# Kernel optimization log

Measured on AMD Instinct MI355X. Metric: run time of the kernel, lower is better.

Reference implementation:

```python
import math
import jax, jax.numpy as jnp
import numpy as np

HID = 1536; H = 8; D = HID // H           # hidden, heads, head_dim
W = 12                                     # chunk (query block) size
L = 13; R = 0                              # context left / right
MAX_PAST = L - 1; MAX_FUT = R
C = W + MAX_PAST + MAX_FUT                 # key context size per block (24)
F = MAX_PAST + MAX_FUT + 1                 # relative span (13)
CAP = 50.0
B, T = 4, 4096


def _timing_signal(positions):
    # positions: [F] float -> [F, HID] sinusoidal embedding
    num_ts = HID // 2
    log_inc = math.log(10000.0) / max(num_ts - 1, 1)
    inv = jnp.exp(jnp.arange(num_ts, dtype=jnp.float32) * -log_inc)
    scaled = positions[:, None] * inv[None, :]
    return jnp.concatenate([jnp.sin(scaled), jnp.cos(scaled)], axis=-1)


def setup_inputs() -> dict:
    key = jax.random.key(0)
    ks = jax.random.split(key, 6)
    s = HID ** -0.5
    return {
        "hidden_states": jax.random.normal(ks[0], (B, T, HID), jnp.float32),
        "mask": jnp.zeros((B, T), bool),  # True = padded/invalid position
        "wq": jax.random.normal(ks[1], (HID, HID), jnp.float32) * s,
        "wk": jax.random.normal(ks[2], (HID, HID), jnp.float32) * s,
        "wv": jax.random.normal(ks[3], (HID, HID), jnp.float32) * s,
        "w_pos": jax.random.normal(ks[4], (HID, HID), jnp.float32) * s,
        "per_dim_scale": jnp.zeros((D,), jnp.float32),
    }


def reference(hidden_states, mask, wq, wk, wv, w_pos, per_dim_scale):
    Bq, Tq, _ = hidden_states.shape
    U = -(-Tq // W)  # number of query blocks
    q = (hidden_states @ wq).reshape(Bq, Tq, H, D)
    k = (hidden_states @ wk).reshape(Bq, Tq, H, D)
    v = (hidden_states @ wv).reshape(Bq, Tq, H, D)
    # q scaling: head_dim**-0.5 / softplus(0) * softplus(per_dim_scale)
    q_scale = (D ** -0.5) / math.log(2.0)
    q = q * (q_scale * jax.nn.softplus(per_dim_scale))
    # query blocks [B, U, W, H, D]
    qb = jnp.pad(q, ((0, 0), (0, U * W - Tq), (0, 0), (0, 0))).reshape(Bq, U, W, H, D)
    # key/value blocks with left/right context [B, U, C, H, D]
    frame_idx = jnp.arange(U)[:, None] * W + jnp.arange(C)[None, :]

    def extract(x):
        pads = ((0, 0), (MAX_PAST, U * W - Tq + MAX_FUT)) + ((0, 0),) * (x.ndim - 2)
        return jnp.pad(x, pads)[:, frame_idx]

    kb = extract(k)
    vb = extract(v)
    valid = extract(~mask)  # [B, U, C] bool, padded frames -> False
    # relative position embedding: projected sinusoid for offsets [MAX_PAST..-MAX_FUT]
    pos = jnp.arange(MAX_PAST, -MAX_FUT - 1, -1, dtype=jnp.float32)  # [F]
    sin_emb = (_timing_signal(pos) @ w_pos).reshape(F, H, D)
    term_ac = jnp.einsum('buwhd,buchd->bhuwc', qb, kb)   # content logits
    term_bd = jnp.einsum('buwhd,fhd->bhuwf', qb, sin_emb)  # position logits (unshifted)
    # Transformer-XL relative shift: pad last dim to C+1, flatten W*(C+1), keep W*C
    tb = jnp.pad(term_bd, ((0, 0),) * 4 + ((0, C + 1 - F),))
    tb = tb.reshape(Bq, H, U, W * (C + 1))[..., :W * C].reshape(Bq, H, U, W, C)
    logits = jnp.tanh((term_ac + tb) / CAP) * CAP
    # local causal validity mask [W, C]
    lower = jnp.tril(jnp.ones((C, W), bool)).T
    upper = jnp.tril(jnp.ones((W, C), bool), k=MAX_PAST + MAX_FUT)
    cond = valid[:, None, :, None, :] & (lower & upper)[None, None, None]
    logits = jnp.where(cond, logits, jnp.float32(np.finfo(np.float32).min))
    probs = jax.nn.softmax(logits, axis=-1)
    ctx = jnp.einsum('bhuwc,buchd->buwhd', probs, vb)
    return ctx.reshape(Bq, U * W, H, D)[:, :Tq]
```

## Files before the change

### kernel.cpp

```cpp
#include <hip/hip_runtime.h>
#include <hip/hip_bf16.h>
#include <cstdint>
#include <cstddef>

typedef __bf16 bf16x8 __attribute__((ext_vector_type(8)));
typedef __bf16 bf16x4_t __attribute__((ext_vector_type(4)));
typedef float f32x4 __attribute__((ext_vector_type(4)));
using bf16_t = __hip_bfloat16;

constexpr int kHID = 1536;
constexpr int kH = 8;
constexpr int kD = 192;
constexpr int kW = 12;
constexpr int kC = 24;
constexpr int kF = 13;
constexpr int kB = 4;
constexpr int kT = 4096;
constexpr int kU = 342;
constexpr int kNQKV = 4608;
constexpr int kM = kB * kT;
constexpr int kKV = 2 * kHID;

constexpr size_t kVtOff = 50331648;
constexpr size_t kWtOff = 100663296;
constexpr size_t kSinOff = kWtOff + (size_t)kNQKV * kHID * 2;
constexpr size_t kSinBfOff = kSinOff + (size_t)kF * kHID * 4;
constexpr size_t kSsOff = kSinBfOff + (size_t)16 * kHID * 2;
constexpr size_t kHsbOff = kSsOff + 1024;
constexpr size_t kQbOff = kHsbOff + (size_t)kM * kHID * 2;
constexpr size_t kWsNeedSmall = kQbOff;
constexpr size_t kWsNeedBig = kQbOff + (size_t)kM * kHID * 2;

__device__ __forceinline__ void load_lds16(const void* g, void* l) {
  __builtin_amdgcn_global_load_lds(
      (const __attribute__((address_space(1))) void*)g,
      (__attribute__((address_space(3))) void*)l, 16, 0, 0);
}

__global__ __launch_bounds__(256) void transpose_w(const float* __restrict__ wq,
                                                   const float* __restrict__ wk,
                                                   const float* __restrict__ wv,
                                                   bf16_t* __restrict__ wt) {
  __shared__ bf16_t tile[32][33];
  const int s = blockIdx.z;
  const float* w = (s == 0) ? wq : (s == 1) ? wk : wv;
  const int k0 = blockIdx.x * 32, n0 = blockIdx.y * 32;
  for (int i = threadIdx.y; i < 32; i += 8)
    tile[i][threadIdx.x] = (bf16_t)w[(size_t)(k0 + i) * kHID + n0 + threadIdx.x];
  __syncthreads();
  for (int i = threadIdx.y; i < 32; i += 8)
    wt[(size_t)(s * kHID + n0 + i) * kHID + k0 + threadIdx.x] = tile[threadIdx.x][i];
}

__global__ __launch_bounds__(256) void convert_hs(const float* __restrict__ hs,
                                                  bf16_t* __restrict__ hsb) {
  const size_t total = (size_t)kM * kHID;
  const size_t stride = (size_t)gridDim.x * 256 * 8;
  for (size_t i = ((size_t)blockIdx.x * 256 + threadIdx.x) * 8; i < total; i += stride) {
    f32x4 a = *(const f32x4*)(hs + i);
    f32x4 b = *(const f32x4*)(hs + i + 4);
    bf16x8 o;
#pragma unroll
    for (int e = 0; e < 4; e++) { o[e] = (__bf16)a[e]; o[e + 4] = (__bf16)b[e]; }
    *(bf16x8*)(hsb + i) = o;
  }
}

__global__ __launch_bounds__(256) void sinemb_kernel(const float* __restrict__ w_pos,
                                                     float* __restrict__ sinb,
                                                     bf16_t* __restrict__ sinbf) {
  __shared__ float ts[kHID];
  const int f = blockIdx.y;
  const int n = blockIdx.x * 256 + threadIdx.x;
  const float pos = (float)(12 - f);
  const float log_inc = logf(10000.0f) / 767.0f;
  for (int j = threadIdx.x; j < 768; j += 256) {
    float inv = expf(-(float)j * log_inc);
    float a = pos * inv;
    ts[j] = sinf(a);
    ts[768 + j] = cosf(a);
  }
  __syncthreads();
  float acc = 0.0f;
  for (int m = 0; m < kHID; m++) acc += ts[m] * w_pos[(size_t)m * kHID + n];
  sinb[f * kHID + n] = acc;
  sinbf[f * kHID + n] = (bf16_t)acc;
  if (f == 0) {
    sinbf[13 * kHID + n] = (bf16_t)0.0f;
    sinbf[14 * kHID + n] = (bf16_t)0.0f;
    sinbf[15 * kHID + n] = (bf16_t)0.0f;
  }
}

__global__ void compute_ss(const float* __restrict__ pds, float* __restrict__ ssb) {
  int d = threadIdx.x;
  if (d < kD) {
    float p = pds[d];
    float sp = log1pf(expf(p));
    ssb[d] = (1.0f / (sqrtf(192.0f) * logf(2.0f))) * sp;
  }
}

template <int MODE>
__global__ __launch_bounds__(256) void gemm_qkv_t(const bf16_t* __restrict__ hsb,
                                                  const bf16_t* __restrict__ wt,
                                                  float* __restrict__ qout,
                                                  bf16_t* __restrict__ kvout,
                                                  bf16_t* __restrict__ vtws,
                                                  bf16_t* __restrict__ qbout,
                                                  const float* __restrict__ ssb) {
  __shared__ bf16_t As[128 * 32];
  __shared__ bf16_t Bs[128 * 32];
  const int tid = threadIdx.x;
  const int lane = tid & 63, wid = tid >> 6;
  const int t0 = blockIdx.y * 128, n0 = blockIdx.x * 128;
  const int mb = lane & 15, quad = lane >> 4;
  const int wrow = (wid >> 1) * 64, wcol = (wid & 1) * 64;

  f32x4 acc[4][4] = {};

  const int c0 = tid, c1 = tid + 256;
  const bf16_t* a0 = hsb + (size_t)(t0 + (c0 >> 2)) * kHID + (c0 & 3) * 8;
  const bf16_t* a1 = hsb + (size_t)(t0 + (c1 >> 2)) * kHID + (c1 & 3) * 8;
  const bf16_t* b0 = wt + (size_t)(n0 + (c0 >> 2)) * kHID + (c0 & 3) * 8;
  const bf16_t* b1 = wt + (size_t)(n0 + (c1 >> 2)) * kHID + (c1 & 3) * 8;
  bf16_t* lA0 = &As[c0 * 8];
  bf16_t* lA1 = &As[c1 * 8];
  bf16_t* lB0 = &Bs[c0 * 8];
  bf16_t* lB1 = &Bs[c1 * 8];

  for (int k0 = 0; k0 < kHID; k0 += 32) {
    __syncthreads();
    load_lds16(a0, lA0);
    load_lds16(a1, lA1);
    load_lds16(b0, lB0);
    load_lds16(b1, lB1);
    a0 += 32; a1 += 32; b0 += 32; b1 += 32;
    __syncthreads();

    bf16x8 af[4], bg[4];
#pragma unroll
    for (int i = 0; i < 4; i++)
      af[i] = *(const bf16x8*)(&As[(wrow + i * 16 + mb) * 32 + quad * 8]);
#pragma unroll
    for (int j = 0; j < 4; j++)
      bg[j] = *(const bf16x8*)(&Bs[(wcol + j * 16 + mb) * 32 + quad * 8]);
#pragma unroll
    for (int i = 0; i < 4; i++)
#pragma unroll
      for (int j = 0; j < 4; j++)
        acc[i][j] = __builtin_amdgcn_mfma_f32_16x16x32_bf16(af[i], bg[j], acc[i][j], 0, 0, 0);
  }

  if constexpr (MODE == 0) {
    const bool isq = (n0 < kHID);
#pragma unroll
    for (int i = 0; i < 4; i++)
#pragma unroll
      for (int j = 0; j < 4; j++)
#pragma unroll
        for (int r = 0; r < 4; r++) {
          int row = t0 + wrow + i * 16 + quad * 4 + r;
          int col = wcol + j * 16 + mb;
          if (isq) {
            qout[(size_t)row * kHID + n0 + col] = acc[i][j][r];
          } else {
            kvout[(size_t)row * kKV + (n0 - kHID) + col] = (bf16_t)acc[i][j][r];
          }
        }
  } else {
    if (n0 < kHID) {
#pragma unroll
      for (int j = 0; j < 4; j++) {
        int colj = n0 + wcol + j * 16 + mb;
        float ssv = ssb[colj % kD];
#pragma unroll
        for (int i = 0; i < 4; i++)
#pragma unroll
          for (int r = 0; r < 4; r++) {
            int row = t0 + wrow + i * 16 + quad * 4 + r;
            qbout[(size_t)row * kHID + colj] = (bf16_t)(acc[i][j][r] * ssv);
          }
      }
    } else if (n0 < 2 * kHID) {
#pragma unroll
      for (int i = 0; i < 4; i++)
#pragma unroll
        for (int j = 0; j < 4; j++)
#pragma unroll
          for (int r = 0; r < 4; r++) {
            int row = t0 + wrow + i * 16 + quad * 4 + r;
            int col = (n0 - kHID) + wcol + j * 16 + mb;
            kvout[(size_t)row * kHID + col] = (bf16_t)acc[i][j][r];
          }
    } else {
#pragma unroll
      for (int i = 0; i < 4; i++)
#pragma unroll
        for (int j = 0; j < 4; j++) {
          int vcol = (n0 - 2 * kHID) + wcol + j * 16 + mb;
          int row = t0 + wrow + i * 16 + quad * 4;
          bf16x4_t vv;
#pragma unroll
          for (int r = 0; r < 4; r++) vv[r] = (__bf16)acc[i][j][r];
          *(bf16x4_t*)(vtws + (size_t)vcol * kM + row) = vv;
        }
    }
  }
}

__global__ __launch_bounds__(256) void attn_mfma(const bf16_t* __restrict__ kvK,
                                                 const bf16_t* __restrict__ vtws,
                                                 const unsigned char* __restrict__ mask,
                                                 const bf16_t* __restrict__ sinbf,
                                                 const bf16_t* __restrict__ qb,
                                                 float* __restrict__ out) {
  const int g = blockIdx.x, b = blockIdx.y, h = blockIdx.z;
  const int tid = threadIdx.x;
  const int lane = tid & 63, wv = tid >> 6;
  const int w = lane & 15, quad = lane >> 4;
  const int tb = g * 48 - 12;
  const int u = g * 4 + wv;

  __shared__ bf16_t Ks[68 * 192];
  __shared__ bf16_t Vt[192 * 80];
  __shared__ __align__(16) char scr[4][1280];
  __shared__ int vld[68];

  float* bdl = (float*)scr[wv];
  bf16_t* Pl = (bf16_t*)scr[wv];

  int tq = u * kW + w;
  int qrow = (u < kU && tq < kT) ? (b * kT + tq) : (b * kT);
  const bf16_t* qptr = qb + (size_t)qrow * kHID + h * kD + quad * 8;
  const bf16_t* sptr = sinbf + (size_t)w * kHID + h * kD + quad * 8;
  bf16x8 qf[6], sf[6];
#pragma unroll
  for (int ks = 0; ks < 6; ks++) {
    qf[ks] = *(const bf16x8*)(qptr + ks * 32);
    sf[ks] = *(const bf16x8*)(sptr + ks * 32);
  }

  if (tid < 68) {
    int p = tb + tid;
    vld[tid] = (p >= 0 && p < kT && mask[b * kT + p] == 0) ? 1 : 0;
  }

  const char* kvb = (const char*)kvK;
#pragma unroll
  for (int it = 0; it < 7; it++) {
    int i = it * 256 + tid;
    if (i >= 1632) i -= 1632;
    int r = i / 24, cb = (i % 24) * 16;
    int row = b * kT + tb + r;
    row = row < 0 ? 0 : (row > kM - 1 ? kM - 1 : row);
    const char* src = kvb + (size_t)row * 3072 + h * 384 + (cb ^ ((r & 7) << 4));
    load_lds16(src, (char*)Ks + i * 16);
  }
  const char* vtb = (const char*)vtws;
#pragma unroll
  for (int it = 0; it < 8; it++) {
    int i = it * 256 + tid;
    if (i >= 1920) i -= 1920;
    int d = i / 10, j = i % 10;
    int e = b * kT + tb - 4 + j * 8;
    e = e < 0 ? 0 : (e > kM - 8 ? kM - 8 : e);
    const char* src = vtb + ((size_t)(h * kD + d) * kM + e) * 2;
    load_lds16(src, (char*)Vt + i * 16);
  }
  __syncthreads();

  f32x4 ac0 = {0.f, 0.f, 0.f, 0.f}, ac1 = {0.f, 0.f, 0.f, 0.f}, bdv = {0.f, 0.f, 0.f, 0.f};
  const int r0 = wv * kW + w;
  const int r1 = r0 + 16;
#pragma unroll
  for (int ks = 0; ks < 6; ks++) {
    int kb = ks * 64 + quad * 16;
    bf16x8 ka0 = *(const bf16x8*)((const char*)Ks + (size_t)r0 * 384 + (kb ^ ((r0 & 7) << 4)));
    bf16x8 ka1 = *(const bf16x8*)((const char*)Ks + (size_t)r1 * 384 + (kb ^ ((r1 & 7) << 4)));
    ac0 = __builtin_amdgcn_mfma_f32_16x16x32_bf16(ka0, qf[ks], ac0, 0, 0, 0);
    ac1 = __builtin_amdgcn_mfma_f32_16x16x32_bf16(ka1, qf[ks], ac1, 0, 0, 0);
    bdv = __builtin_amdgcn_mfma_f32_16x16x32_bf16(sf[ks], qf[ks], bdv, 0, 0, 0);
  }

  *(f32x4*)&bdl[w * 16 + quad * 4] = bdv;
  asm volatile("s_waitcnt lgkmcnt(0)" ::: "memory");

  float l[8];
#pragma unroll
  for (int T = 0; T < 2; T++)
#pragma unroll
    for (int r = 0; r < 4; r++) {
      int c = T * 16 + quad * 4 + r;
      int f = c - w;
      int fr = f < 0 ? 0 : (f > 15 ? 15 : f);
      float a = T ? ac1[r] : ac0[r];
      float bb = bdl[w * 16 + fr];
      bool val = (f >= 0) && (f <= 12) && (c < kC) && (vld[wv * kW + c] != 0);
      float x2 = (a + bb) * 0.04f;
      float ee = __expf(x2);
      float th = (ee - 1.0f) * __builtin_amdgcn_rcpf(ee + 1.0f);
      l[T * 4 + r] = val ? 50.0f * th : -3.4028234663852886e38f;
    }

  float m = l[0];
#pragma unroll
  for (int k = 1; k < 8; k++) m = fmaxf(m, l[k]);
  m = fmaxf(m, __shfl_xor(m, 16, 64));
  m = fmaxf(m, __shfl_xor(m, 32, 64));
  float e8[8], s = 0.0f;
#pragma unroll
  for (int k = 0; k < 8; k++) { e8[k] = __expf(l[k] - m); s += e8[k]; }
  s += __shfl_xor(s, 16, 64);
  s += __shfl_xor(s, 32, 64);
  float inv = 1.0f / s;

#pragma unroll
  for (int T = 0; T < 2; T++) {
    bf16x4_t pk;
#pragma unroll
    for (int r = 0; r < 4; r++) {
      int c = T * 16 + quad * 4 + r;
      float p = (c < kC) ? e8[T * 4 + r] * inv : 0.0f;
      pk[r] = (__bf16)p;
    }
    *(bf16x4_t*)&Pl[w * 40 + T * 16 + quad * 4] = pk;
  }
  asm volatile("s_waitcnt lgkmcnt(0)" ::: "memory");
  __builtin_amdgcn_sched_barrier(0);

  bf16x8 pa = *(const bf16x8*)&Pl[w * 40 + quad * 8];
  const int cl0 = 4 + wv * kW + quad * 8;
  const bool uok = (u < kU);
#pragma unroll
  for (int T = 0; T < 12; T++) {
    bf16x4_t v0 = *(const bf16x4_t*)&Vt[(T * 16 + w) * 80 + cl0];
    bf16x4_t v1 = *(const bf16x4_t*)&Vt[(T * 16 + w) * 80 + cl0 + 4];
    bf16x8 vf;
#pragma unroll
    for (int e2 = 0; e2 < 4; e2++) { vf[e2] = v0[e2]; vf[e2 + 4] = v1[e2]; }
    f32x4 oz = {0.f, 0.f, 0.f, 0.f};
    oz = __builtin_amdgcn_mfma_f32_16x16x32_bf16(pa, vf, oz, 0, 0, 0);
    if (uok) {
#pragma unroll
      for (int r = 0; r < 4; r++) {
        int wr = quad * 4 + r;
        int t = u * kW + wr;
        if (wr < kW && t < kT)
          out[((size_t)(b * kT + t)) * kHID + h * kD + T * 16 + w] = oz[r];
      }
    }
  }
}

__global__ __launch_bounds__(256) void attn_kernel(const bf16_t* __restrict__ kv,
                                                   const unsigned char* __restrict__ mask,
                                                   const float* __restrict__ sinb,
                                                   const float* __restrict__ pds,
                                                   float* __restrict__ out) {
  const int u = blockIdx.x, b = blockIdx.y, h = blockIdx.z;
  const int tid = threadIdx.x;

  __shared__ float qs[kW][kD + 1];
  __shared__ float ks[kC][kD + 1];
  __shared__ float vs[kC][kD + 1];
  __shared__ float sins[kF][kD + 1];
  __shared__ float lg[kW][kC + 1];
  __shared__ float ss[kD];
  __shared__ int validc[kC];

  if (tid < kD) {
    float p = pds[tid];
    float sp = log1pf(expf(p));
    ss[tid] = (1.0f / (sqrtf(192.0f) * logf(2.0f))) * sp;
  }
  if (tid < kC) {
    int p = u * kW + tid - 12;
    validc[tid] = (p >= 0 && p < kT && mask[b * kT + p] == 0) ? 1 : 0;
  }
  __syncthreads();

  for (int i = tid; i < kW * kD; i += 256) {
    int w = i / kD, d = i % kD;
    int t = u * kW + w;
    float v = 0.0f;
    if (t < kT) v = out[((size_t)(b * kT + t)) * kHID + h * kD + d] * ss[d];
    qs[w][d] = v;
  }
  for (int i = tid; i < kC * kD; i += 256) {
    int c = i / kD, d = i % kD;
    int p = u * kW + c - 12;
    float kval = 0.0f, vval = 0.0f;
    if (p >= 0 && p < kT) {
      size_t base = (size_t)(b * kT + p) * kKV;
      kval = (float)kv[base + h * kD + d];
      vval = (float)kv[base + kHID + h * kD + d];
    }
    ks[c][d] = kval;
    vs[c][d] = vval;
  }
  for (int i = tid; i < kF * kD; i += 256) {
    int f = i / kD, d = i % kD;
    sins[f][d] = sinb[f * kHID + h * kD + d];
  }
  __syncthreads();

  for (int i = tid; i < kW * kC; i += 256) {
    int w = i / kC, c = i % kC;
    float l = -3.4028234663852886e38f;
    int f = c - w;
    if (f >= 0 && f <= 12 && validc[c]) {
      float ac = 0.0f, bd = 0.0f;
      for (int d = 0; d < kD; d++) {
        float q = qs[w][d];
        ac += q * ks[c][d];
        bd += q * sins[f][d];
      }
      l = tanhf((ac + bd) * (1.0f / 50.0f)) * 50.0f;
    }
    lg[w][c] = l;
  }
  __syncthreads();

  if (tid < kW) {
    float m = -3.4028234663852886e38f;
#pragma unroll
    for (int c = 0; c < kC; c++) m = fmaxf(m, lg[tid][c]);
    float e[kC];
    float s = 0.0f;
#pragma unroll
    for (int c = 0; c < kC; c++) {
      float ex = expf(lg[tid][c] - m);
      e[c] = ex;
      s += ex;
    }
    float inv = 1.0f / s;
#pragma unroll
    for (int c = 0; c < kC; c++) lg[tid][c] = e[c] * inv;
  }
  __syncthreads();

  for (int i = tid; i < kW * kD; i += 256) {
    int w = i / kD, d = i % kD;
    int t = u * kW + w;
    if (t >= kT) continue;
    float acc = 0.0f;
#pragma unroll
    for (int c = 0; c < 13; c++) acc += lg[w][w + c] * vs[w + c][d];
    out[((size_t)(b * kT + t)) * kHID + h * kD + d] = acc;
  }
}

extern "C" void kernel_launch(void* const* d_in, const int* in_sizes, int n_in,
                              void* d_out, int out_size, void* d_ws, size_t ws_size,
                              hipStream_t stream) {
  if (ws_size < kWsNeedSmall) return;

  const float* hs = (const float*)d_in[0];
  const unsigned char* mask = (const unsigned char*)d_in[1];
  const float* wq = (const float*)d_in[2];
  const float* wk = (const float*)d_in[3];
  const float* wv = (const float*)d_in[4];
  const float* wpos = (const float*)d_in[5];
  const float* pds = (const float*)d_in[6];
  float* out = (float*)d_out;

  char* ws = (char*)d_ws;
  bf16_t* kvK = (bf16_t*)ws;
  bf16_t* vtws = (bf16_t*)(ws + kVtOff);
  bf16_t* wt = (bf16_t*)(ws + kWtOff);
  float* sinb = (float*)(ws + kSinOff);
  bf16_t* sinbf = (bf16_t*)(ws + kSinBfOff);
  float* ssb = (float*)(ws + kSsOff);
  bf16_t* hsb = (bf16_t*)(ws + kHsbOff);
  bf16_t* qb = (bf16_t*)(ws + kQbOff);

  const bool big = ws_size >= kWsNeedBig;

  transpose_w<<<dim3(48, 48, 3), dim3(32, 8), 0, stream>>>(wq, wk, wv, wt);
  convert_hs<<<dim3(2048), 256, 0, stream>>>(hs, hsb);
  sinemb_kernel<<<dim3(6, 13), 256, 0, stream>>>(wpos, sinb, sinbf);
  compute_ss<<<1, 192, 0, stream>>>(pds, ssb);

  if (big) {
    gemm_qkv_t<1><<<dim3(kNQKV / 128, kM / 128), 256, 0, stream>>>(
        hsb, wt, nullptr, kvK, vtws, qb, ssb);
    attn_mfma<<<dim3(86, kB, kH), 256, 0, stream>>>(kvK, vtws, mask, sinbf, qb, out);
  } else {
    gemm_qkv_t<0><<<dim3(kNQKV / 128, kM / 128), 256, 0, stream>>>(
        hsb, wt, out, kvK, nullptr, nullptr, nullptr);
    attn_kernel<<<dim3(kU, kB, kH), 256, 0, stream>>>(kvK, mask, sinb, pds, out);
  }
}
```

Baseline: 611.7 us.

## Add 256x256-tile QKV GEMM with 128KB LDS and split-K sinusoid projection

Adds a new QKV projection GEMM that uses 256x256 output tiles, 512 threads, 128KB of dynamic LDS, swizzled async LDS staging and double buffering. Larger tiles raise arithmetic intensity and cut how often operands are reloaded from global memory. It falls back to the old 128-tile GEMM if the attribute set or launch fails. Separately, the serial 1536-step sinusoid-embedding matvec is split across 12 K-chunks (written temporarily into the output buffer) followed by a reduce kernel, which adds parallelism to that small stage.

```diff
diff --git a/kernel.cpp b/kernel.cpp
--- a/kernel.cpp
+++ b/kernel.cpp
@@ -85,6 +85,52 @@
   for (int m = 0; m < kHID; m++) acc += ts[m] * w_pos[(size_t)m * kHID + n];
   sinb[f * kHID + n] = acc;
   sinbf[f * kHID + n] = (bf16_t)acc;
+  if (f == 0) {
+    sinbf[13 * kHID + n] = (bf16_t)0.0f;
+    sinbf[14 * kHID + n] = (bf16_t)0.0f;
+    sinbf[15 * kHID + n] = (bf16_t)0.0f;
+  }
+}
+
+__global__ __launch_bounds__(256) void sinemb_part(const float* __restrict__ w_pos,
+                                                   float* __restrict__ sinp) {
+  __shared__ float tsL[kF][128];
+  const int nc = blockIdx.x;
+  const int ms = blockIdx.y;
+  const int tid = threadIdx.x;
+  const float log_inc = logf(10000.0f) / 767.0f;
+  for (int i = tid; i < kF * 128; i += 256) {
+    int f = i >> 7, ml = i & 127;
+    int m = ms * 128 + ml;
+    float pos = (float)(12 - f);
+    float v;
+    if (m < 768) v = sinf(pos * expf(-(float)m * log_inc));
+    else v = cosf(pos * expf(-(float)(m - 768) * log_inc));
+    tsL[f][ml] = v;
+  }
+  __syncthreads();
+  const int n = nc * 256 + tid;
+  float acc[kF] = {};
+  for (int ml = 0; ml < 128; ml++) {
+    float wp = w_pos[(size_t)(ms * 128 + ml) * kHID + n];
+#pragma unroll
+    for (int f = 0; f < kF; f++) acc[f] += tsL[f][ml] * wp;
+  }
+#pragma unroll
+  for (int f = 0; f < kF; f++) sinp[((size_t)ms * kF + f) * kHID + n] = acc[f];
+}
+
+__global__ __launch_bounds__(256) void sinemb_reduce(const float* __restrict__ sinp,
+                                                     float* __restrict__ sinb,
+                                                     bf16_t* __restrict__ sinbf) {
+  int i = blockIdx.x * 256 + threadIdx.x;
+  if (i >= kF * kHID) return;
+  int f = i / kHID, n = i % kHID;
+  float s = 0.0f;
+#pragma unroll
+  for (int ms = 0; ms < 12; ms++) s += sinp[((size_t)ms * kF + f) * kHID + n];
+  sinb[i] = s;
+  sinbf[i] = (bf16_t)s;
   if (f == 0) {
     sinbf[13 * kHID + n] = (bf16_t)0.0f;
     sinbf[14 * kHID + n] = (bf16_t)0.0f;
@@ -209,6 +255,159 @@
   }
 }
 
+__global__ __launch_bounds__(512, 2) void gemm256(const bf16_t* __restrict__ hsb,
+                                                  const bf16_t* __restrict__ wt,
+                                                  bf16_t* __restrict__ kvout,
+                                                  bf16_t* __restrict__ vtws,
+                                                  bf16_t* __restrict__ qbout,
+                                                  const float* __restrict__ ssb) {
+  extern __shared__ __align__(16) char sm[];
+  const int tid = threadIdx.x;
+  const int lane = tid & 63;
+  const int wid = tid >> 6;
+  const int mb = lane & 15, quad = lane >> 4;
+  const int wm = wid >> 2, wn = wid & 3;
+  const int t0 = blockIdx.y * 256, n0 = blockIdx.x * 256;
+
+  const int i0 = tid, i1 = tid + 512;
+  const int r0 = i0 >> 2, cs0 = (i0 & 3) ^ ((r0 >> 2) & 3);
+  const int r1 = i1 >> 2, cs1 = (i1 & 3) ^ ((r1 >> 2) & 3);
+  const bf16_t* aS0 = hsb + (size_t)(t0 + r0) * kHID + cs0 * 8;
+  const bf16_t* aS1 = hsb + (size_t)(t0 + r1) * kHID + cs1 * 8;
+  const bf16_t* bS0 = wt + (size_t)(n0 + r0) * kHID + cs0 * 8;
+  const bf16_t* bS1 = wt + (size_t)(n0 + r1) * kHID + cs1 * 8;
+
+#define AH(buf, kh) (sm + (buf) * 32768 + (kh) * 16384)
+#define BH(buf, kh) (sm + 65536 + (buf) * 32768 + (kh) * 16384)
+#define STAGE_A(buf, kh, kt) do { int ko_ = (kt) * 64 + (kh) * 32; \
+    load_lds16(aS0 + ko_, AH(buf, kh) + i0 * 16); \
+    load_lds16(aS1 + ko_, AH(buf, kh) + i1 * 16); } while (0)
+#define STAGE_B(buf, kh, kt) do { int ko_ = (kt) * 64 + (kh) * 32; \
+    load_lds16(bS0 + ko_, BH(buf, kh) + i0 * 16); \
+    load_lds16(bS1 + ko_, BH(buf, kh) + i1 * 16); } while (0)
+
+  const int sw16 = (quad ^ ((mb >> 2) & 3)) * 16;
+  const int aRow = wm * 128 + mb;
+  const int bRow = wn * 64 + mb;
+
+  f32x4 acc[8][4] = {};
+  bf16x8 af[4], bfr[4];
+
+  STAGE_A(0, 0, 0); STAGE_B(0, 0, 0); STAGE_A(0, 1, 0); STAGE_B(0, 1, 0);
+
+  for (int kt = 0; kt < 24; kt++) {
+    const int cur = kt & 1, nxt = cur ^ 1;
+    const int ktn = (kt < 23) ? kt + 1 : 23;
+    const char* Ac0 = AH(cur, 0); const char* Bc0 = BH(cur, 0);
+    const char* Ac1 = AH(cur, 1); const char* Bc1 = BH(cur, 1);
+
+    STAGE_A(nxt, 0, ktn);
+    asm volatile("s_waitcnt vmcnt(6)" ::: "memory");
+    __builtin_amdgcn_s_barrier();
+    __builtin_amdgcn_sched_barrier(0);
+#pragma unroll
+    for (int x = 0; x < 4; x++)
+      af[x] = *(const bf16x8*)(Ac0 + (size_t)(aRow + x * 16) * 64 + sw16);
+#pragma unroll
+    for (int x = 0; x < 4; x++)
+      bfr[x] = *(const bf16x8*)(Bc0 + (size_t)(bRow + x * 16) * 64 + sw16);
+    __builtin_amdgcn_s_setprio(1);
+#pragma unroll
+    for (int i = 0; i < 4; i++)
+#pragma unroll
+      for (int j = 0; j < 4; j++)
+        acc[i][j] = __builtin_amdgcn_mfma_f32_16x16x32_bf16(af[i], bfr[j], acc[i][j], 0, 0, 0);
+    __builtin_amdgcn_s_setprio(0);
+
+    STAGE_B(nxt, 0, ktn);
+#pragma unroll
+    for (int x = 0; x < 4; x++)
+      af[x] = *(const bf16x8*)(Ac0 + (size_t)(aRow + 64 + x * 16) * 64 + sw16);
+    __builtin_amdgcn_s_setprio(1);
+#pragma unroll
+    for (int i = 0; i < 4; i++)
+#pragma unroll
+      for (int j = 0; j < 4; j++)
+        acc[4 + i][j] = __builtin_amdgcn_mfma_f32_16x16x32_bf16(af[i], bfr[j], acc[4 + i][j], 0, 0, 0);
+    __builtin_amdgcn_s_setprio(0);
+
+    STAGE_A(nxt, 1, ktn);
+    asm volatile("s_waitcnt vmcnt(6)" ::: "memory");
+    __builtin_amdgcn_s_barrier();
+    __builtin_amdgcn_sched_barrier(0);
+#pragma unroll
+    for (int x = 0; x < 4; x++)
+      af[x] = *(const bf16x8*)(Ac1 + (size_t)(aRow + x * 16) * 64 + sw16);
+#pragma unroll
+    for (int x = 0; x < 4; x++)
+      bfr[x] = *(const bf16x8*)(Bc1 + (size_t)(bRow + x * 16) * 64 + sw16);
+    __builtin_amdgcn_s_setprio(1);
+#pragma unroll
+    for (int i = 0; i < 4; i++)
+#pragma unroll
+      for (int j = 0; j < 4; j++)
+        acc[i][j] = __builtin_amdgcn_mfma_f32_16x16x32_bf16(af[i], bfr[j], acc[i][j], 0, 0, 0);
+    __builtin_amdgcn_s_setprio(0);
+
+    STAGE_B(nxt, 1, ktn);
+#pragma unroll
+    for (int x = 0; x < 4; x++)
+      af[x] = *(const bf16x8*)(Ac1 + (size_t)(aRow + 64 + x * 16) * 64 + sw16);
+    __builtin_amdgcn_s_setprio(1);
+#pragma unroll
+    for (int i = 0; i < 4; i++)
+#pragma unroll
+      for (int j = 0; j < 4; j++)
+        acc[4 + i][j] = __builtin_amdgcn_mfma_f32_16x16x32_bf16(af[i], bfr[j], acc[4 + i][j], 0, 0, 0);
+    __builtin_amdgcn_s_setprio(0);
+
+    __builtin_amdgcn_s_barrier();
+    __builtin_amdgcn_sched_barrier(0);
+  }
+#undef AH
+#undef BH
+#undef STAGE_A
+#undef STAGE_B
+
+  if (n0 < kHID) {
+#pragma unroll
+    for (int j = 0; j < 4; j++) {
+      int colj = n0 + wn * 64 + j * 16 + mb;
+      float ssv = ssb[colj % kD];
+#pragma unroll
+      for (int i = 0; i < 8; i++)
+#pragma unroll
+        for (int r = 0; r < 4; r++) {
+          int row = t0 + wm * 128 + i * 16 + quad * 4 + r;
+          qbout[(size_t)row * kHID + colj] = (bf16_t)(acc[i][j][r] * ssv);
+        }
+    }
+  } else if (n0 < 2 * kHID) {
+#pragma unroll
+    for (int i = 0; i < 8; i++)
+#pragma unroll
+      for (int j = 0; j < 4; j++)
+#pragma unroll
+        for (int r = 0; r < 4; r++) {
+          int row = t0 + wm * 128 + i * 16 + quad * 4 + r;
+          int col = (n0 - kHID) + wn * 64 + j * 16 + mb;
+          kvout[(size_t)row * kHID + col] = (bf16_t)acc[i][j][r];
+        }
+  } else {
+#pragma unroll
+    for (int i = 0; i < 8; i++)
+#pragma unroll
+      for (int j = 0; j < 4; j++) {
+        int vcol = (n0 - 2 * kHID) + wn * 64 + j * 16 + mb;
+        int row = t0 + wm * 128 + i * 16 + quad * 4;
+        bf16x4_t vv;
+#pragma unroll
+        for (int r = 0; r < 4; r++) vv[r] = (__bf16)acc[i][j][r];
+        *(bf16x4_t*)(vtws + (size_t)vcol * kM + row) = vv;
+      }
+  }
+}
+
 __global__ __launch_bounds__(256) void attn_mfma(const bf16_t* __restrict__ kvK,
                                                  const bf16_t* __restrict__ vtws,
                                                  const unsigned char* __restrict__ mask,
@@ -477,16 +676,39 @@
 
   const bool big = ws_size >= kWsNeedBig;
 
+  static int g_big_lds = -1;
+  if (g_big_lds < 0) {
+    g_big_lds = (hipFuncSetAttribute((const void*)gemm256,
+                                     hipFuncAttributeMaxDynamicSharedMemorySize,
+                                     131072) == hipSuccess) ? 1 : 0;
+  }
+
   transpose_w<<<dim3(48, 48, 3), dim3(32, 8), 0, stream>>>(wq, wk, wv, wt);
   convert_hs<<<dim3(2048), 256, 0, stream>>>(hs, hsb);
-  sinemb_kernel<<<dim3(6, 13), 256, 0, stream>>>(wpos, sinb, sinbf);
   compute_ss<<<1, 192, 0, stream>>>(pds, ssb);
 
   if (big) {
-    gemm_qkv_t<1><<<dim3(kNQKV / 128, kM / 128), 256, 0, stream>>>(
-        hsb, wt, nullptr, kvK, vtws, qb, ssb);
+    float* sinp = (float*)d_out;
+    sinemb_part<<<dim3(6, 12), 256, 0, stream>>>(wpos, sinp);
+    sinemb_reduce<<<dim3(78), 256, 0, stream>>>(sinp, sinb, sinbf);
+    bool ran256 = false;
+    if (g_big_lds) {
+      (void)hipGetLastError();
+      gemm256<<<dim3(kNQKV / 256, kM / 256), 512, 131072, stream>>>(
+          hsb, wt, kvK, vtws, qb, ssb);
+      if (hipGetLastError() == hipSuccess) {
+        ran256 = true;
+      } else {
+        g_big_lds = 0;
+      }
+    }
+    if (!ran256) {
+      gemm_qkv_t<1><<<dim3(kNQKV / 128, kM / 128), 256, 0, stream>>>(
+          hsb, wt, nullptr, kvK, vtws, qb, ssb);
+    }
     attn_mfma<<<dim3(86, kB, kH), 256, 0, stream>>>(kvK, vtws, mask, sinbf, qb, out);
   } else {
+    sinemb_kernel<<<dim3(6, 13), 256, 0, stream>>>(wpos, sinb, sinbf);
     gemm_qkv_t<0><<<dim3(kNQKV / 128, kM / 128), 256, 0, stream>>>(
         hsb, wt, out, kvK, nullptr, nullptr, nullptr);
     attn_kernel<<<dim3(kU, kB, kH), 256, 0, stream>>>(kvK, mask, sinb, pds, out);
```

After: 551.7 us. 1.11x faster.
